# Kernel tuning notes

Hardware: AMD Instinct MI355X
Metric: run time of the kernel (lower is better)

Reference implementation:

```python
import jax, jax.numpy as jnp
import numpy as np


def setup_inputs() -> dict:
    key = jax.random.key(0)
    k1, k2, k3, k4 = jax.random.split(key, 4)
    B, S, IN, OUT = 4, 2048, 4096, 11008
    x = jax.random.normal(k1, (B, S, IN), dtype=jnp.float32)
    # int8 symmetric weights stored as int8 (values in [-127, 127])
    weight = jax.random.randint(k2, (OUT, IN), -127, 128, dtype=jnp.int32).astype(jnp.int8)
    # per-output-channel scale, small positive values
    weight_scale = jax.random.uniform(k3, (OUT, 1), dtype=jnp.float32) * 0.01
    bias = jax.random.normal(k4, (OUT,), dtype=jnp.float32)
    return {"x": x, "weight": weight, "weight_scale": weight_scale, "bias": bias}


def reference(x, weight, weight_scale, bias):
    # dequant: int8 weight * per-row scale -> [out, in] in x's dtype
    dequant_weight = weight.astype(weight_scale.dtype) * weight_scale
    # F.linear: x @ W^T + b
    out = jnp.einsum('bsi,oi->bso', x, dequant_weight)
    return out + bias
```

## Files before the change

kernel.cpp:

```cpp
#include <hip/hip_runtime.h>
#include <hip/hip_bf16.h>
#include <stdint.h>


#define M_DIM 8192
#define K_DIM 4096
#define N_DIM 11008

#define BM 128
#define BN 128
#define BK 32

#define TBM 256
#define TBN 256
#define TBK 64

typedef __attribute__((ext_vector_type(8))) short short8;
typedef __attribute__((ext_vector_type(4))) float floatx4;

__device__ __forceinline__ unsigned short f2bf(float f) {
    __hip_bfloat16 h = __float2bfloat16(f);
    return __builtin_bit_cast(unsigned short, h);
}

__global__ void cvt_x(const float* __restrict__ x, unsigned short* __restrict__ o) {
    int i = (blockIdx.x * 256 + threadIdx.x) * 8;
    float4 a = *(const float4*)(x + i);
    float4 b = *(const float4*)(x + i + 4);
    union { unsigned short h[8]; uint4 v; } u;
    u.h[0] = f2bf(a.x); u.h[1] = f2bf(a.y); u.h[2] = f2bf(a.z); u.h[3] = f2bf(a.w);
    u.h[4] = f2bf(b.x); u.h[5] = f2bf(b.y); u.h[6] = f2bf(b.z); u.h[7] = f2bf(b.w);
    *(uint4*)(o + i) = u.v;
}

__global__ void cvt_w(const int* __restrict__ w, unsigned short* __restrict__ o) {
    int i = (blockIdx.x * 256 + threadIdx.x) * 8;
    int4 a = *(const int4*)(w + i);
    int4 b = *(const int4*)(w + i + 4);
    union { unsigned short h[8]; uint4 v; } u;
    u.h[0] = f2bf((float)a.x); u.h[1] = f2bf((float)a.y);
    u.h[2] = f2bf((float)a.z); u.h[3] = f2bf((float)a.w);
    u.h[4] = f2bf((float)b.x); u.h[5] = f2bf((float)b.y);
    u.h[6] = f2bf((float)b.z); u.h[7] = f2bf((float)b.w);
    *(uint4*)(o + i) = u.v;
}


#define BARX()  __builtin_amdgcn_s_barrier()
#define LGKM0() asm volatile("s_waitcnt lgkmcnt(0)" ::: "memory")
#define VM4()   asm volatile("s_waitcnt vmcnt(4)" ::: "memory")
#define PHI()   __builtin_amdgcn_s_setprio(1)
#define PLO()   __builtin_amdgcn_s_setprio(0)

#define STAGE(GP, LP)                                                              \
    do {                                                                           \
        __builtin_amdgcn_global_load_lds(                                          \
            (const __attribute__((address_space(1))) void*)((GP) + so0),           \
            (__attribute__((address_space(3))) void*)((LP) + tid * 8), 16, 0, 0);  \
        __builtin_amdgcn_global_load_lds(                                          \
            (const __attribute__((address_space(1))) void*)((GP) + so1),           \
            (__attribute__((address_space(3))) void*)((LP) + 4096 + tid * 8), 16, 0, 0); \
    } while (0)

#define LDA4(BASE, MOFF)                                                           \
    do {                                                                           \
        _Pragma("unroll")                                                          \
        for (int m_ = 0; m_ < 4; ++m_)                                             \
            _Pragma("unroll")                                                      \
            for (int ks_ = 0; ks_ < 2; ++ks_)                                      \
                af[m_][ks_] = *(const short8*)((BASE) +                            \
                    ((wm * 128 + ((MOFF) + m_) * 16 + fr) * 128 +                  \
                     ((ks_ * 64 + fk16) ^ sxor)));                                 \
    } while (0)

#define LDB2(BASE, N0)                                                             \
    do {                                                                           \
        _Pragma("unroll")                                                          \
        for (int n_ = 0; n_ < 2; ++n_)                                             \
            _Pragma("unroll")                                                      \
            for (int ks_ = 0; ks_ < 2; ++ks_)                                      \
                bf[(N0) + n_][ks_] = *(const short8*)((BASE) +                     \
                    ((wn * 64 + ((N0) + n_) * 16 + fr) * 128 +                     \
                     ((ks_ * 64 + fk16) ^ sxor)));                                 \
    } while (0)

#define MFMAQ(MOFF, NOFF, BOFF)                                                    \
    do {                                                                           \
        _Pragma("unroll")                                                          \
        for (int m_ = 0; m_ < 4; ++m_)                                             \
            _Pragma("unroll")                                                      \
            for (int n_ = 0; n_ < 2; ++n_)                                         \
                _Pragma("unroll")                                                  \
                for (int ks_ = 0; ks_ < 2; ++ks_)                                  \
                    acc[(MOFF) + m_][(NOFF) + n_] =                                \
                        __builtin_amdgcn_mfma_f32_16x16x32_bf16(                   \
                            af[m_][ks_], bf[(BOFF) + n_][ks_],                     \
                            acc[(MOFF) + m_][(NOFF) + n_], 0, 0, 0);               \
    } while (0)

__global__ __launch_bounds__(512, 2) void gemm8(
    const unsigned short* __restrict__ A,
    const unsigned short* __restrict__ B,
    const float* __restrict__ scale,
    const float* __restrict__ bias,
    float* __restrict__ C) {
    __shared__ unsigned short sh[4 * 16384];
    unsigned short* A0 = sh;
    unsigned short* B0 = sh + 16384;
    unsigned short* A1 = sh + 32768;
    unsigned short* B1 = sh + 49152;

    const int tid  = threadIdx.x;
    const int lane = tid & 63;
    const int wave = tid >> 6;
    const int wm = wave & 1;
    const int wn = wave >> 1;

    const int cpx = ((M_DIM / TBM) * (N_DIM / TBN)) >> 3;
    const int wg  = (blockIdx.x & 7) * cpx + (blockIdx.x >> 3);
    const int bm  = wg & 31;
    const int bn  = wg >> 5;

    const unsigned short* Apan = A + (size_t)bm * TBM * K_DIM;
    const unsigned short* Bpan = B + (size_t)bn * TBN * K_DIM;

    const int li0 = tid, li1 = tid + 512;
    const size_t so0 = (size_t)(li0 >> 3) * K_DIM +
                       (size_t)((((li0 & 7) ^ (((li0 >> 5) & 1) << 1))) * 8);
    const size_t so1 = (size_t)(li1 >> 3) * K_DIM +
                       (size_t)((((li1 & 7) ^ (((li1 >> 5) & 1) << 1))) * 8);
    const size_t HALF1 = (size_t)128 * K_DIM;

    const int fr   = lane & 15;
    const int fk16 = (lane >> 4) * 16;
    const int sxor = ((fr >> 2) & 1) << 5;

    const char* A0c = (const char*)A0;
    const char* B0c = (const char*)B0;
    const char* A1c = (const char*)A1;
    const char* B1c = (const char*)B1;

    floatx4 acc[8][4] = {};
    short8 af[4][2], bf[4][2];

    STAGE(Apan,              A0);
    STAGE(Apan + HALF1,      A0 + 8192);
    STAGE(Bpan,              B0);
    STAGE(Bpan + HALF1,      B0 + 8192);
    STAGE(Bpan + 64,         B1);
    STAGE(Bpan + HALF1 + 64, B1 + 8192);
    VM4();
    BARX();

    for (int i = 0; i < K_DIM / TBK / 2; ++i) {
        const int kt1 = 2 * i + 1;
        const int kt2 = (2 * i + 2 < 64) ? 2 * i + 2 : 63;
        const int kt3 = (2 * i + 3 < 64) ? 2 * i + 3 : 63;

        LDA4(A0c, 0); LDB2(B0c, 0);
        STAGE(Apan + (size_t)kt1 * 64, A1);
        BARX(); LGKM0(); PHI(); MFMAQ(0, 0, 0); PLO(); BARX();

        LDB2(B0c, 2);
        STAGE(Apan + HALF1 + (size_t)kt1 * 64, A1 + 8192);
        BARX(); LGKM0(); PHI(); MFMAQ(0, 2, 2); PLO(); BARX();

        LDA4(A0c, 4);
        STAGE(Bpan + (size_t)kt2 * 64, B0);
        BARX(); LGKM0(); PHI(); MFMAQ(4, 2, 2); PLO(); BARX();

        STAGE(Bpan + HALF1 + (size_t)kt2 * 64, B0 + 8192);
        VM4();
        BARX(); LGKM0(); PHI(); MFMAQ(4, 0, 0); PLO(); BARX();

        LDA4(A1c, 0); LDB2(B1c, 0);
        STAGE(Apan + (size_t)kt2 * 64, A0);
        BARX(); LGKM0(); PHI(); MFMAQ(0, 0, 0); PLO(); BARX();

        LDB2(B1c, 2);
        STAGE(Apan + HALF1 + (size_t)kt2 * 64, A0 + 8192);
        BARX(); LGKM0(); PHI(); MFMAQ(0, 2, 2); PLO(); BARX();

        LDA4(A1c, 4);
        STAGE(Bpan + (size_t)kt3 * 64, B1);
        BARX(); LGKM0(); PHI(); MFMAQ(4, 2, 2); PLO(); BARX();

        STAGE(Bpan + HALF1 + (size_t)kt3 * 64, B1 + 8192);
        VM4();
        BARX(); LGKM0(); PHI(); MFMAQ(4, 0, 0); PLO(); BARX();
    }

    const int cm = (lane >> 4) * 4;
    const int cn = lane & 15;
#pragma unroll
    for (int ni = 0; ni < 4; ++ni) {
        const int gn = bn * TBN + wn * 64 + ni * 16 + cn;
        const float s  = scale[gn];
        const float bb = bias[gn];
#pragma unroll
        for (int mi = 0; mi < 8; ++mi) {
            const int gm0 = bm * TBM + wm * 128 + mi * 16 + cm;
#pragma unroll
            for (int r = 0; r < 4; ++r)
                C[(size_t)(gm0 + r) * N_DIM + gn] = acc[mi][ni][r] * s + bb;
        }
    }
}

__global__ __launch_bounds__(256) void gemm_fused(
    const float* __restrict__ X, const int* __restrict__ W,
    const float* __restrict__ scale, const float* __restrict__ bias,
    float* __restrict__ C) {
    __shared__ unsigned short As[BM * BK];
    __shared__ unsigned short Bs[BN * BK];
    const int tid = threadIdx.x;
    const int lane = tid & 63, wave = tid >> 6;
    const int wm = wave & 1, wn = wave >> 1;
    const int bm = blockIdx.x, bn = blockIdx.y;
    floatx4 acc[4][4] = {};
    const int srow = tid >> 1;
    const int scol = (tid & 1) * 16;
    const float* xp = X + (size_t)(bm * BM + srow) * K_DIM + scol;
    const int*   wp = W + (size_t)(bn * BN + srow) * K_DIM + scol;
    const int fr = lane & 15, fk = (lane >> 4) * 8;

    for (int k0 = 0; k0 < K_DIM; k0 += BK) {
        union { float4 v[4]; float f[16]; } fx;
        union { int4 v[4]; int s[16]; } fw;
#pragma unroll
        for (int i = 0; i < 4; ++i) fx.v[i] = *(const float4*)(xp + k0 + i * 4);
#pragma unroll
        for (int i = 0; i < 4; ++i) fw.v[i] = *(const int4*)(wp + k0 + i * 4);
        union { unsigned short h[16]; uint4 v[2]; } ha, hb;
#pragma unroll
        for (int i = 0; i < 16; ++i) ha.h[i] = f2bf(fx.f[i]);
#pragma unroll
        for (int i = 0; i < 16; ++i) hb.h[i] = f2bf((float)fw.s[i]);
        __syncthreads();
        *(uint4*)(As + srow * BK + scol)     = ha.v[0];
        *(uint4*)(As + srow * BK + scol + 8) = ha.v[1];
        *(uint4*)(Bs + srow * BK + scol)     = hb.v[0];
        *(uint4*)(Bs + srow * BK + scol + 8) = hb.v[1];
        __syncthreads();

        short8 a_f[4], b_f[4];
#pragma unroll
        for (int i = 0; i < 4; ++i)
            a_f[i] = *(const short8*)(As + (wm * 64 + i * 16 + fr) * BK + fk);
#pragma unroll
        for (int i = 0; i < 4; ++i)
            b_f[i] = *(const short8*)(Bs + (wn * 64 + i * 16 + fr) * BK + fk);
#pragma unroll
        for (int mi = 0; mi < 4; ++mi)
#pragma unroll
            for (int ni = 0; ni < 4; ++ni)
                acc[mi][ni] = __builtin_amdgcn_mfma_f32_16x16x32_bf16(
                    a_f[mi], b_f[ni], acc[mi][ni], 0, 0, 0);
    }

    const int cm = (lane >> 4) * 4;
    const int cn = lane & 15;
#pragma unroll
    for (int ni = 0; ni < 4; ++ni) {
        int gn = bn * BN + wn * 64 + ni * 16 + cn;
        float s = scale[gn], bb = bias[gn];
#pragma unroll
        for (int mi = 0; mi < 4; ++mi) {
            int gm0 = bm * BM + wm * 64 + mi * 16 + cm;
#pragma unroll
            for (int r = 0; r < 4; ++r)
                C[(size_t)(gm0 + r) * N_DIM + gn] = acc[mi][ni][r] * s + bb;
        }
    }
}

extern "C" void kernel_launch(void* const* d_in, const int* in_sizes, int n_in,
                              void* d_out, int out_size, void* d_ws, size_t ws_size,
                              hipStream_t stream) {
    const float* x     = (const float*)d_in[0];
    const int*   w     = (const int*)d_in[1];
    const float* scale = (const float*)d_in[2];
    const float* bias  = (const float*)d_in[3];
    float* out = (float*)d_out;

    const size_t a_elems = (size_t)M_DIM * K_DIM;
    const size_t b_elems = (size_t)N_DIM * K_DIM;
    const size_t need = (a_elems + b_elems) * sizeof(unsigned short);

    if (ws_size >= need) {
        unsigned short* xa = (unsigned short*)d_ws;
        unsigned short* wb = xa + a_elems;
        cvt_x<<<(int)(a_elems / 2048), 256, 0, stream>>>(x, xa);
        cvt_w<<<(int)(b_elems / 2048), 256, 0, stream>>>(w, wb);
        const int nwg = (M_DIM / TBM) * (N_DIM / TBN);
        gemm8<<<dim3(nwg), dim3(512), 0, stream>>>(xa, wb, scale, bias, out);
    } else {
        dim3 grid(M_DIM / BM, N_DIM / BN);
        gemm_fused<<<grid, 256, 0, stream>>>(x, w, scale, bias, out);
    }
}
```

Measured before the change: 1.268 ms.

## Use full 8-way XOR LDS swizzle and XCD-local block-to-tile mapping

Replaces the partial XOR swizzle on the LDS staging layout with a full 3-bit row-based XOR over the eight 16-byte chunks. The fragment read offsets are recomputed to match, removing LDS bank conflicts on the short8 reads. It also remaps workgroups so that each XCD owns a contiguous group of four M-tiles across N, which should improve L2 reuse of the A panel. The new mapping is only valid for the 32x43 tile grid, and the write and read swizzles must stay consistent.

```diff
diff --git a/kernel.cpp b/kernel.cpp
--- a/kernel.cpp
+++ b/kernel.cpp
@@ -65,23 +65,21 @@
 #define LDA4(BASE, MOFF)                                                           \
     do {                                                                           \
         _Pragma("unroll")                                                          \
-        for (int m_ = 0; m_ < 4; ++m_)                                             \
-            _Pragma("unroll")                                                      \
-            for (int ks_ = 0; ks_ < 2; ++ks_)                                      \
-                af[m_][ks_] = *(const short8*)((BASE) +                            \
-                    ((wm * 128 + ((MOFF) + m_) * 16 + fr) * 128 +                  \
-                     ((ks_ * 64 + fk16) ^ sxor)));                                 \
+        for (int m_ = 0; m_ < 4; ++m_) {                                           \
+            const int r_ = (wm * 128 + ((MOFF) + m_) * 16 + fr) * 128;             \
+            af[m_][0] = *(const short8*)((BASE) + r_ + col0);                      \
+            af[m_][1] = *(const short8*)((BASE) + r_ + col1);                      \
+        }                                                                          \
     } while (0)
 
 #define LDB2(BASE, N0)                                                             \
     do {                                                                           \
         _Pragma("unroll")                                                          \
-        for (int n_ = 0; n_ < 2; ++n_)                                             \
-            _Pragma("unroll")                                                      \
-            for (int ks_ = 0; ks_ < 2; ++ks_)                                      \
-                bf[(N0) + n_][ks_] = *(const short8*)((BASE) +                     \
-                    ((wn * 64 + ((N0) + n_) * 16 + fr) * 128 +                     \
-                     ((ks_ * 64 + fk16) ^ sxor)));                                 \
+        for (int n_ = 0; n_ < 2; ++n_) {                                           \
+            const int r_ = (wn * 64 + ((N0) + n_) * 16 + fr) * 128;                \
+            bf[(N0) + n_][0] = *(const short8*)((BASE) + r_ + col0);               \
+            bf[(N0) + n_][1] = *(const short8*)((BASE) + r_ + col1);               \
+        }                                                                          \
     } while (0)
 
 #define MFMAQ(MOFF, NOFF, BOFF)                                                    \
@@ -116,24 +114,24 @@
     const int wm = wave & 1;
     const int wn = wave >> 1;
 
-    const int cpx = ((M_DIM / TBM) * (N_DIM / TBN)) >> 3;
-    const int wg  = (blockIdx.x & 7) * cpx + (blockIdx.x >> 3);
-    const int bm  = wg & 31;
-    const int bn  = wg >> 5;
+    const int xcd = blockIdx.x & 7;
+    const int sq  = blockIdx.x >> 3;
+    const int bm  = xcd * 4 + (sq & 3);
+    const int bn  = sq >> 2;
 
     const unsigned short* Apan = A + (size_t)bm * TBM * K_DIM;
     const unsigned short* Bpan = B + (size_t)bn * TBN * K_DIM;
 
     const int li0 = tid, li1 = tid + 512;
     const size_t so0 = (size_t)(li0 >> 3) * K_DIM +
-                       (size_t)((((li0 & 7) ^ (((li0 >> 5) & 1) << 1))) * 8);
+                       (size_t)(((li0 & 7) ^ ((li0 >> 3) & 7)) * 8);
     const size_t so1 = (size_t)(li1 >> 3) * K_DIM +
-                       (size_t)((((li1 & 7) ^ (((li1 >> 5) & 1) << 1))) * 8);
+                       (size_t)(((li1 & 7) ^ ((li1 >> 3) & 7)) * 8);
     const size_t HALF1 = (size_t)128 * K_DIM;
 
     const int fr   = lane & 15;
-    const int fk16 = (lane >> 4) * 16;
-    const int sxor = ((fr >> 2) & 1) << 5;
+    const int col0 = (((lane >> 4) ^ (fr & 7)) << 4);
+    const int col1 = col0 ^ 64;
 
     const char* A0c = (const char*)A0;
     const char* B0c = (const char*)B0;
```

Measured after the change: 1.159 ms. 8.6% less time.
